# Performance work log

Measured on AMD Instinct MI355X. Metric: run time of the kernel, lower is better.

The kernel has to match this reference:

```python
import jax, jax.numpy as jnp
import numpy as np

B, CAP, H, NH = 128, 65536, 512, 8
HD = H // NH
GH = H // 4  # gate hidden


def setup_inputs() -> dict:
    key = jax.random.key(0)
    ks = jax.random.split(key, 8)
    s = 1.0 / np.sqrt(H)
    sg = 1.0 / np.sqrt(GH)
    return {
        "query": jax.random.normal(ks[0], (B, H), jnp.float32),
        "memory_keys": jax.random.normal(ks[1], (CAP, H), jnp.float32) * s,
        "memory_values": jax.random.normal(ks[2], (CAP, H), jnp.float32) * s,
        "in_proj_w": jax.random.normal(ks[3], (3 * H, H), jnp.float32) * s,
        "in_proj_b": jnp.zeros((3 * H,), jnp.float32),
        "out_proj_w": jax.random.normal(ks[4], (H, H), jnp.float32) * s,
        "out_proj_b": jnp.zeros((H,), jnp.float32),
        "gate_w1": jax.random.normal(ks[5], (GH, H), jnp.float32) * s,
        "gate_b1": jnp.zeros((GH,), jnp.float32),
        "gate_w2": jax.random.normal(ks[6], (1, GH), jnp.float32) * sg,
        "gate_b2": jnp.zeros((1,), jnp.float32),
        "usage_count": jnp.zeros((CAP,), jnp.float32),
        "last_used": jnp.zeros((CAP,), jnp.float32),
        "step_counter": 1,
    }


def reference(query, memory_keys, memory_values, in_proj_w, in_proj_b,
              out_proj_w, out_proj_b, gate_w1, gate_b1, gate_w2, gate_b2,
              usage_count, last_used, step_counter):
    # nn.MultiheadAttention packed projections: rows [0:H]=Wq, [H:2H]=Wk, [2H:3H]=Wv
    wq, wk, wv = in_proj_w[:H], in_proj_w[H:2 * H], in_proj_w[2 * H:]
    bq, bk, bv = in_proj_b[:H], in_proj_b[H:2 * H], in_proj_b[2 * H:]

    q = (query @ wq.T + bq).reshape(B, NH, HD)           # [B, h, d] (q_len = 1)
    k = (memory_keys @ wk.T + bk).reshape(CAP, NH, HD)   # [C, h, d]
    v = (memory_values @ wv.T + bv).reshape(CAP, NH, HD)  # [C, h, d]

    scores = jnp.einsum('bhd,chd->bhc', q, k) / np.sqrt(HD)  # [B, h, C]
    attn = jax.nn.softmax(scores, axis=-1)
    ctx = jnp.einsum('bhc,chd->bhd', attn, v).reshape(B, H)
    attn_out = ctx @ out_proj_w.T + out_proj_b               # [B, H]

    # usage bookkeeping: attn_weights averaged over heads, then over batch
    avg_attn = attn.mean(axis=(0, 1))                        # [C]
    new_usage = usage_count + avg_attn
    new_last = jnp.where(avg_attn > 1e-3,
                         jnp.float32(step_counter), last_used)

    # gating MLP: Linear -> ReLU -> Linear -> Sigmoid
    gate = jax.nn.sigmoid(
        jax.nn.relu(query @ gate_w1.T + gate_b1) @ gate_w2.T + gate_b2)  # [B, 1]
    memory_output = gate * attn_out                          # [B, H]
    return memory_output, new_usage, new_last
```

## Files before the change

### kernel.cpp

```cpp
#include <hip/hip_runtime.h>
#include <stdint.h>


typedef __bf16 b16x8 __attribute__((ext_vector_type(8)));
typedef float f32x4 __attribute__((ext_vector_type(4)));

static __device__ __forceinline__ unsigned short f2bf(float f) {
  unsigned int u = __float_as_uint(f);
  u = (u + 0x7FFFu + ((u >> 16) & 1u)) >> 16;
  return (unsigned short)u;
}

static __device__ __forceinline__ f32x4 MFMA(b16x8 a, b16x8 b, f32x4 c) {
  return __builtin_amdgcn_mfma_f32_16x16x32_bf16(a, b, c, 0, 0, 0);
}

__global__ void k_convert_w(const float* __restrict__ w, unsigned short* __restrict__ dst) {
  int i = blockIdx.x * 256 + threadIdx.x;
  float4 v = reinterpret_cast<const float4*>(w + 512 * 512)[i];
  ushort4 o;
  o.x = f2bf(v.x); o.y = f2bf(v.y); o.z = f2bf(v.z); o.w = f2bf(v.w);
  reinterpret_cast<ushort4*>(dst)[i] = o;
}

__global__ void k_proj_q(const float* __restrict__ query, const float* __restrict__ w,
                         const float* __restrict__ bias, unsigned short* __restrict__ qout) {
  __shared__ float qs[512];
  int b = blockIdx.x, j = threadIdx.x;
  qs[j] = query[b * 512 + j];
  __syncthreads();
  float acc = bias[j];
  const float4* q4 = reinterpret_cast<const float4*>(qs);
  const float4* w4 = reinterpret_cast<const float4*>(w + j * 512);
#pragma unroll 8
  for (int i = 0; i < 128; ++i) {
    float4 a = q4[i], c = w4[i];
    acc += a.x * c.x + a.y * c.y + a.z * c.z + a.w * c.w;
  }
  qout[b * 512 + j] = f2bf(acc);
}

__global__ void k_gate(const float* __restrict__ query, const float* __restrict__ w1,
                       const float* __restrict__ b1, const float* __restrict__ w2,
                       const float* __restrict__ b2, float* __restrict__ gate) {
  __shared__ float qs[512];
  __shared__ float red[2];
  int b = blockIdx.x, j = threadIdx.x;
  qs[j] = query[b * 512 + j];
  qs[j + 128] = query[b * 512 + j + 128];
  qs[j + 256] = query[b * 512 + j + 256];
  qs[j + 384] = query[b * 512 + j + 384];
  __syncthreads();
  float acc = b1[j];
  const float4* q4 = reinterpret_cast<const float4*>(qs);
  const float4* w4 = reinterpret_cast<const float4*>(w1 + j * 512);
#pragma unroll 8
  for (int i = 0; i < 128; ++i) {
    float4 a = q4[i], c = w4[i];
    acc += a.x * c.x + a.y * c.y + a.z * c.z + a.w * c.w;
  }
  float t = fmaxf(acc, 0.f) * w2[j];
#pragma unroll
  for (int off = 1; off < 64; off <<= 1) t += __shfl_xor(t, off, 64);
  if ((j & 63) == 0) red[j >> 6] = t;
  __syncthreads();
  if (j == 0) {
    float z = red[0] + red[1] + b2[0];
    gate[b] = 1.f / (1.f + __builtin_amdgcn_exp2f(-z * 1.44269504088896f));
  }
}

__global__ __launch_bounds__(512) void k_proj_kv(
    const float* __restrict__ mk, const float* __restrict__ mv,
    const unsigned short* __restrict__ wkb, const unsigned short* __restrict__ wvb,
    const float* __restrict__ in_b,
    unsigned short* __restrict__ kout, unsigned short* __restrict__ vtout) {
  const int isV = blockIdx.y;
  const float* A = isV ? mv : mk;
  const unsigned short* W = isV ? wvb : wkb;
  const float* bias = in_b + (isV ? 1024 : 512);
  const int c0 = blockIdx.x * 64;
  const int tid = threadIdx.x;
  const int w = tid >> 6, ln = tid & 15, g = (tid & 63) >> 4;
  __shared__ __align__(16) unsigned short Al[64 * 32];
  __shared__ __align__(16) unsigned short Wl[512 * 32];

  f32x4 acc[4][4];
#pragma unroll
  for (int m = 0; m < 4; ++m)
#pragma unroll
    for (int n = 0; n < 4; ++n) acc[m][n] = {0.f, 0.f, 0.f, 0.f};

  for (int kk = 0; kk < 16; ++kk) {
    {
      int row = tid >> 3, c4 = (tid & 7) << 2;
      float4 v = *reinterpret_cast<const float4*>(&A[(size_t)(c0 + row) * 512 + kk * 32 + c4]);
      ushort4 o;
      o.x = f2bf(v.x); o.y = f2bf(v.y); o.z = f2bf(v.z); o.w = f2bf(v.w);
      *reinterpret_cast<ushort4*>(&Al[row * 32 + c4]) = o;
    }
#pragma unroll
    for (int i = 0; i < 4; ++i) {
      int fc = i * 512 + tid, row = fc >> 2, part = fc & 3;
      *reinterpret_cast<uint4*>(&Wl[row * 32 + part * 8]) =
          *reinterpret_cast<const uint4*>(&W[(size_t)row * 512 + kk * 32 + part * 8]);
    }
    __syncthreads();
    b16x8 a[4], bb[4];
#pragma unroll
    for (int m = 0; m < 4; ++m)
      a[m] = *reinterpret_cast<const b16x8*>(&Al[(16 * m + ln) * 32 + g * 8]);
#pragma unroll
    for (int n = 0; n < 4; ++n)
      bb[n] = *reinterpret_cast<const b16x8*>(&Wl[(64 * w + 16 * n + ln) * 32 + g * 8]);
#pragma unroll
    for (int m = 0; m < 4; ++m)
#pragma unroll
      for (int n = 0; n < 4; ++n) acc[m][n] = MFMA(a[m], bb[n], acc[m][n]);
    __syncthreads();
  }
  float bj[4];
#pragma unroll
  for (int n = 0; n < 4; ++n) bj[n] = bias[64 * w + 16 * n + ln];
#pragma unroll
  for (int m = 0; m < 4; ++m)
#pragma unroll
    for (int n = 0; n < 4; ++n) {
      int j = 64 * w + 16 * n + ln;
#pragma unroll
      for (int r = 0; r < 4; ++r) {
        int c = c0 + 16 * m + 4 * g + r;
        unsigned short val = f2bf(acc[m][n][r] + bj[n]);
        if (!isV) kout[(size_t)c * 512 + j] = val;
        else      vtout[(size_t)j * 65536 + c] = val;
      }
    }
}

__global__ __launch_bounds__(256) void k_attn1(
    const unsigned short* __restrict__ kb, const unsigned short* __restrict__ vt,
    const unsigned short* __restrict__ qb,
    float* __restrict__ l_ws, float* __restrict__ ctxT) {
  const int h = blockIdx.y, cg = blockIdx.x;
  const int tid = threadIdx.x;
  const int wv = tid >> 6, wr = wv >> 1, wc = wv & 1;
  const int ln = tid & 15, g = (tid & 63) >> 4;
  __shared__ __align__(16) unsigned short kS[128 * 64];
  __shared__ __align__(16) unsigned short pS[128 * 128];
  __shared__ __align__(16) unsigned short vS[64 * 128];
  const float SC = 0.125f * 1.44269504088896f;

  b16x8 qf[4][2];
#pragma unroll
  for (int n = 0; n < 4; ++n)
#pragma unroll
    for (int ks = 0; ks < 2; ++ks) {
      int b = 64 * wc + 16 * n + ln;
      qf[n][ks] = *reinterpret_cast<const b16x8*>(&qb[(size_t)b * 512 + h * 64 + ks * 32 + g * 8]);
    }
  f32x4 pacc[2][4];
#pragma unroll
  for (int m = 0; m < 2; ++m)
#pragma unroll
    for (int n = 0; n < 4; ++n) pacc[m][n] = {0.f, 0.f, 0.f, 0.f};
  float lsum[4] = {0.f, 0.f, 0.f, 0.f};

  for (int it = 0; it < 8; ++it) {
    int c0g = cg * 1024 + it * 128;
#pragma unroll
    for (int i = 0; i < 4; ++i) {
      int fl = i * 256 + tid, row = fl >> 3, p8 = fl & 7;
      uint4 d = *reinterpret_cast<const uint4*>(&kb[(size_t)(c0g + row) * 512 + h * 64 + p8 * 8]);
      *reinterpret_cast<uint4*>(&kS[(row * 8 + (p8 ^ (row & 7))) * 8]) = d;
    }
#pragma unroll
    for (int i = 0; i < 4; ++i) {
      int fl = i * 256 + tid, row = fl >> 4, p16 = fl & 15;
      uint4 d = *reinterpret_cast<const uint4*>(&vt[(size_t)(h * 64 + row) * 65536 + c0g + p16 * 8]);
      *reinterpret_cast<uint4*>(&vS[(row * 16 + (p16 ^ (row & 7))) * 8]) = d;
    }
    __syncthreads();

    f32x4 sacc[4][4];
#pragma unroll
    for (int m = 0; m < 4; ++m)
#pragma unroll
      for (int n = 0; n < 4; ++n) sacc[m][n] = {0.f, 0.f, 0.f, 0.f};
#pragma unroll
    for (int ks = 0; ks < 2; ++ks) {
      b16x8 a[4];
#pragma unroll
      for (int m = 0; m < 4; ++m) {
        int row = 64 * wr + 16 * m + ln;
        a[m] = *reinterpret_cast<const b16x8*>(&kS[(row * 8 + ((ks * 4 + g) ^ (row & 7))) * 8]);
      }
#pragma unroll
      for (int m = 0; m < 4; ++m)
#pragma unroll
        for (int n = 0; n < 4; ++n) sacc[m][n] = MFMA(a[m], qf[n][ks], sacc[m][n]);
    }
#pragma unroll
    for (int m = 0; m < 4; ++m)
#pragma unroll
      for (int n = 0; n < 4; ++n) {
        float p0 = __builtin_amdgcn_exp2f(sacc[m][n][0] * SC);
        float p1 = __builtin_amdgcn_exp2f(sacc[m][n][1] * SC);
        float p2 = __builtin_amdgcn_exp2f(sacc[m][n][2] * SC);
        float p3 = __builtin_amdgcn_exp2f(sacc[m][n][3] * SC);
        lsum[n] += (p0 + p1) + (p2 + p3);
        int b = 64 * wc + 16 * n + ln;
        int c = 64 * wr + 16 * m + 4 * g;
        int base = b * 128 + (((c >> 3) ^ (b & 7)) * 8) + (c & 7);
        ushort2 lo, hi;
        lo.x = f2bf(p0); lo.y = f2bf(p1);
        hi.x = f2bf(p2); hi.y = f2bf(p3);
        *reinterpret_cast<ushort2*>(&pS[base]) = lo;
        *reinterpret_cast<ushort2*>(&pS[base + 2]) = hi;
      }
    __syncthreads();
#pragma unroll
    for (int ks = 0; ks < 4; ++ks) {
      b16x8 av[2], bp[4];
#pragma unroll
      for (int m = 0; m < 2; ++m) {
        int row = 32 * wr + 16 * m + ln;
        av[m] = *reinterpret_cast<const b16x8*>(&vS[(row * 16 + ((ks * 4 + g) ^ (row & 7))) * 8]);
      }
#pragma unroll
      for (int n = 0; n < 4; ++n) {
        int row = 64 * wc + 16 * n + ln;
        bp[n] = *reinterpret_cast<const b16x8*>(&pS[(row * 16 + ((ks * 4 + g) ^ (row & 7))) * 8]);
      }
#pragma unroll
      for (int m = 0; m < 2; ++m)
#pragma unroll
        for (int n = 0; n < 4; ++n) pacc[m][n] = MFMA(av[m], bp[n], pacc[m][n]);
    }
    __syncthreads();
  }
#pragma unroll
  for (int n = 0; n < 4; ++n) {
    float v = lsum[n];
    v += __shfl_xor(v, 16, 64);
    v += __shfl_xor(v, 32, 64);
    if ((tid & 63) < 16) atomicAdd(&l_ws[h * 128 + 64 * wc + 16 * n + ln], v);
  }
#pragma unroll
  for (int m = 0; m < 2; ++m)
#pragma unroll
    for (int n = 0; n < 4; ++n)
#pragma unroll
      for (int r = 0; r < 4; ++r) {
        int d = 32 * wr + 16 * m + 4 * g + r;
        int b = 64 * wc + 16 * n + ln;
        atomicAdd(&ctxT[(h * 64 + d) * 128 + b], pacc[m][n][r]);
      }
}

__global__ __launch_bounds__(256) void k_attn2(
    const unsigned short* __restrict__ kb, const unsigned short* __restrict__ qb,
    const float* __restrict__ l_ws, float* __restrict__ avgA) {
  const int h = blockIdx.y, cg = blockIdx.x;
  const int tid = threadIdx.x;
  const int wv = tid >> 6, wr = wv >> 1, wc = wv & 1;
  const int ln = tid & 15, g = (tid & 63) >> 4;
  __shared__ __align__(16) unsigned short kS[128 * 64];
  __shared__ float wS[128];
  const float SC = 0.125f * 1.44269504088896f;
  if (tid < 128) wS[tid] = 1.f / l_ws[h * 128 + tid];
  b16x8 qf[4][2];
#pragma unroll
  for (int n = 0; n < 4; ++n)
#pragma unroll
    for (int ks = 0; ks < 2; ++ks) {
      int b = 64 * wc + 16 * n + ln;
      qf[n][ks] = *reinterpret_cast<const b16x8*>(&qb[(size_t)b * 512 + h * 64 + ks * 32 + g * 8]);
    }
  __syncthreads();
  float wn[4];
#pragma unroll
  for (int n = 0; n < 4; ++n) wn[n] = wS[64 * wc + 16 * n + ln];

  for (int it = 0; it < 8; ++it) {
    int c0g = cg * 1024 + it * 128;
#pragma unroll
    for (int i = 0; i < 4; ++i) {
      int fl = i * 256 + tid, row = fl >> 3, p8 = fl & 7;
      uint4 d = *reinterpret_cast<const uint4*>(&kb[(size_t)(c0g + row) * 512 + h * 64 + p8 * 8]);
      *reinterpret_cast<uint4*>(&kS[(row * 8 + (p8 ^ (row & 7))) * 8]) = d;
    }
    __syncthreads();
    f32x4 sacc[4][4];
#pragma unroll
    for (int m = 0; m < 4; ++m)
#pragma unroll
      for (int n = 0; n < 4; ++n) sacc[m][n] = {0.f, 0.f, 0.f, 0.f};
#pragma unroll
    for (int ks = 0; ks < 2; ++ks) {
      b16x8 a[4];
#pragma unroll
      for (int m = 0; m < 4; ++m) {
        int row = 64 * wr + 16 * m + ln;
        a[m] = *reinterpret_cast<const b16x8*>(&kS[(row * 8 + ((ks * 4 + g) ^ (row & 7))) * 8]);
      }
#pragma unroll
      for (int m = 0; m < 4; ++m)
#pragma unroll
        for (int n = 0; n < 4; ++n) sacc[m][n] = MFMA(a[m], qf[n][ks], sacc[m][n]);
    }
#pragma unroll
    for (int m = 0; m < 4; ++m) {
      float s0 = 0.f, s1 = 0.f, s2 = 0.f, s3 = 0.f;
#pragma unroll
      for (int n = 0; n < 4; ++n) {
        s0 += __builtin_amdgcn_exp2f(sacc[m][n][0] * SC) * wn[n];
        s1 += __builtin_amdgcn_exp2f(sacc[m][n][1] * SC) * wn[n];
        s2 += __builtin_amdgcn_exp2f(sacc[m][n][2] * SC) * wn[n];
        s3 += __builtin_amdgcn_exp2f(sacc[m][n][3] * SC) * wn[n];
      }
#pragma unroll
      for (int off = 1; off < 16; off <<= 1) {
        s0 += __shfl_xor(s0, off, 64);
        s1 += __shfl_xor(s1, off, 64);
        s2 += __shfl_xor(s2, off, 64);
        s3 += __shfl_xor(s3, off, 64);
      }
      if (ln == 0) {
        int c = c0g + 64 * wr + 16 * m + 4 * g;
        atomicAdd(&avgA[c], s0);
        atomicAdd(&avgA[c + 1], s1);
        atomicAdd(&avgA[c + 2], s2);
        atomicAdd(&avgA[c + 3], s3);
      }
    }
    __syncthreads();
  }
}

__global__ void k_finalize(const float* __restrict__ ctxT, const float* __restrict__ l_ws,
                           const float* __restrict__ wout, const float* __restrict__ bout,
                           const float* __restrict__ gate, float* __restrict__ out) {
  __shared__ float cs[512];
  int b = blockIdx.x, j = threadIdx.x;
  cs[j] = ctxT[j * 128 + b] / l_ws[(j >> 6) * 128 + b];
  __syncthreads();
  float acc = bout[j];
  const float4* c4 = reinterpret_cast<const float4*>(cs);
  const float4* w4 = reinterpret_cast<const float4*>(wout + j * 512);
#pragma unroll 8
  for (int i = 0; i < 128; ++i) {
    float4 a = c4[i], c = w4[i];
    acc += a.x * c.x + a.y * c.y + a.z * c.z + a.w * c.w;
  }
  out[b * 512 + j] = gate[b] * acc;
}

__global__ void k_usage(const float* __restrict__ avgA, const float* __restrict__ usage,
                        const float* __restrict__ last, const int* __restrict__ step,
                        float* __restrict__ out_usage, float* __restrict__ out_last) {
  int c = blockIdx.x * 256 + threadIdx.x;
  float avg = avgA[c] * (1.f / 1024.f);
  out_usage[c] = usage[c] + avg;
  out_last[c] = (avg > 0.001f) ? (float)step[0] : last[c];
}

extern "C" void kernel_launch(void* const* d_in, const int* in_sizes, int n_in,
                              void* d_out, int out_size, void* d_ws, size_t ws_size,
                              hipStream_t stream) {
  const float* query = (const float*)d_in[0];
  const float* mk    = (const float*)d_in[1];
  const float* mv    = (const float*)d_in[2];
  const float* in_w  = (const float*)d_in[3];
  const float* in_b  = (const float*)d_in[4];
  const float* out_w = (const float*)d_in[5];
  const float* out_b = (const float*)d_in[6];
  const float* gw1   = (const float*)d_in[7];
  const float* gb1   = (const float*)d_in[8];
  const float* gw2   = (const float*)d_in[9];
  const float* gb2   = (const float*)d_in[10];
  const float* usage = (const float*)d_in[11];
  const float* last  = (const float*)d_in[12];
  const int*   step  = (const int*)d_in[13];

  char* ws = (char*)d_ws;
  unsigned short* qb  = (unsigned short*)(ws);
  unsigned short* wkb = (unsigned short*)(ws + 131072);
  unsigned short* wvb = (unsigned short*)(ws + 655360);
  unsigned short* kb  = (unsigned short*)(ws + 1179648);
  unsigned short* vt  = (unsigned short*)(ws + 68288512);
  float* l_ws = (float*)(ws + 135397376);
  float* ctxT = (float*)(ws + 135401472);
  float* avgA = (float*)(ws + 135663616);
  float* gate = (float*)(ws + 135925760);
  float* out = (float*)d_out;

  hipMemsetAsync(ws + 135397376, 0, 4096 + 262144 + 262144, stream);

  k_convert_w<<<512, 256, 0, stream>>>(in_w, wkb);
  k_proj_q<<<128, 512, 0, stream>>>(query, in_w, in_b, qb);
  k_gate<<<128, 128, 0, stream>>>(query, gw1, gb1, gw2, gb2, gate);
  k_proj_kv<<<dim3(1024, 2), 512, 0, stream>>>(mk, mv, wkb, wvb, in_b, kb, vt);
  k_attn1<<<dim3(64, 8), 256, 0, stream>>>(kb, vt, qb, l_ws, ctxT);
  k_attn2<<<dim3(64, 8), 256, 0, stream>>>(kb, qb, l_ws, avgA);
  k_finalize<<<128, 512, 0, stream>>>(ctxT, l_ws, out_w, out_b, gate, out);
  k_usage<<<256, 256, 0, stream>>>(avgA, usage, last, step, out + 65536, out + 131072);
}
```

Baseline: 413.3 us.

## Retile K/V projection into 128x128 tiles with direct-to-LDS weight loads and swizzle

The K/V projection GEMM now uses 128x128 output tiles with 256 threads instead of 64 rows by the full 512 columns with 512 threads. Weight tiles are loaded straight into LDS with global_load_lds, and both LDS tiles use an XOR swizzle to avoid bank conflicts. The transposed V output is written as 4-element vector stores. The memory rows are now re-read and re-converted once per column tile (4x), trading extra fp32 input traffic for smaller LDS use and higher occupancy.

```diff
diff --git a/kernel.cpp b/kernel.cpp
--- a/kernel.cpp
+++ b/kernel.cpp
@@ -4,6 +4,7 @@
 
 typedef __bf16 b16x8 __attribute__((ext_vector_type(8)));
 typedef float f32x4 __attribute__((ext_vector_type(4)));
+typedef unsigned short u16x8 __attribute__((ext_vector_type(8)));
 
 static __device__ __forceinline__ unsigned short f2bf(float f) {
   unsigned int u = __float_as_uint(f);
@@ -14,6 +15,11 @@
 static __device__ __forceinline__ f32x4 MFMA(b16x8 a, b16x8 b, f32x4 c) {
   return __builtin_amdgcn_mfma_f32_16x16x32_bf16(a, b, c, 0, 0, 0);
 }
+
+#define GLL16(g, l)                                                          \
+  __builtin_amdgcn_global_load_lds(                                          \
+      (const __attribute__((address_space(1))) void*)(g),                    \
+      (__attribute__((address_space(3))) void*)(l), 16, 0, 0)
 
 __global__ void k_convert_w(const float* __restrict__ w, unsigned short* __restrict__ dst) {
   int i = blockIdx.x * 256 + threadIdx.x;
@@ -70,20 +76,24 @@
   }
 }
 
-__global__ __launch_bounds__(512) void k_proj_kv(
+__global__ __launch_bounds__(256) void k_proj_kv(
     const float* __restrict__ mk, const float* __restrict__ mv,
     const unsigned short* __restrict__ wkb, const unsigned short* __restrict__ wvb,
     const float* __restrict__ in_b,
     unsigned short* __restrict__ kout, unsigned short* __restrict__ vtout) {
-  const int isV = blockIdx.y;
-  const float* A = isV ? mv : mk;
+  const int isV = blockIdx.z;
+  const float* Ag = isV ? mv : mk;
   const unsigned short* W = isV ? wvb : wkb;
   const float* bias = in_b + (isV ? 1024 : 512);
-  const int c0 = blockIdx.x * 64;
+  const int j0 = blockIdx.x * 128;
+  const int c0 = blockIdx.y * 128;
   const int tid = threadIdx.x;
-  const int w = tid >> 6, ln = tid & 15, g = (tid & 63) >> 4;
-  __shared__ __align__(16) unsigned short Al[64 * 32];
-  __shared__ __align__(16) unsigned short Wl[512 * 32];
+  const int wv = tid >> 6, wr = wv >> 1, wc = wv & 1;
+  const int ln = tid & 15, g = (tid & 63) >> 4;
+  const int sw = (ln >> 1) & 3;
+
+  __shared__ __align__(16) unsigned short Al[128 * 32];
+  __shared__ __align__(16) unsigned short Wl[128 * 32];
 
   f32x4 acc[4][4];
 #pragma unroll
@@ -91,48 +101,73 @@
 #pragma unroll
     for (int n = 0; n < 4; ++n) acc[m][n] = {0.f, 0.f, 0.f, 0.f};
 
+  const int arow = tid >> 1, ah = tid & 1;
+  const float* aptr = Ag + (size_t)(c0 + arow) * 512 + ah * 16;
+  const int s_a = (arow >> 1) & 3;
+  unsigned short* awr0 = &Al[arow * 32 + (((2 * ah) ^ s_a) << 3)];
+  unsigned short* awr1 = &Al[arow * 32 + (((2 * ah + 1) ^ s_a) << 3)];
+
+  const int r0 = tid >> 2, p0 = (tid & 3) ^ ((r0 >> 1) & 3);
+  const int r1 = 64 + (tid >> 2), p1 = (tid & 3) ^ ((r1 >> 1) & 3);
+  const unsigned short* wsrc0 = W + (size_t)(j0 + r0) * 512 + p0 * 8;
+  const unsigned short* wsrc1 = W + (size_t)(j0 + r1) * 512 + p1 * 8;
+  unsigned short* wdst0 = &Wl[(wv << 6) * 8];
+  unsigned short* wdst1 = &Wl[(256 + (wv << 6)) * 8];
+
   for (int kk = 0; kk < 16; ++kk) {
-    {
-      int row = tid >> 3, c4 = (tid & 7) << 2;
-      float4 v = *reinterpret_cast<const float4*>(&A[(size_t)(c0 + row) * 512 + kk * 32 + c4]);
-      ushort4 o;
-      o.x = f2bf(v.x); o.y = f2bf(v.y); o.z = f2bf(v.z); o.w = f2bf(v.w);
-      *reinterpret_cast<ushort4*>(&Al[row * 32 + c4]) = o;
-    }
-#pragma unroll
-    for (int i = 0; i < 4; ++i) {
-      int fc = i * 512 + tid, row = fc >> 2, part = fc & 3;
-      *reinterpret_cast<uint4*>(&Wl[row * 32 + part * 8]) =
-          *reinterpret_cast<const uint4*>(&W[(size_t)row * 512 + kk * 32 + part * 8]);
-    }
-    __syncthreads();
-    b16x8 a[4], bb[4];
+    GLL16(wsrc0 + kk * 32, wdst0);
+    GLL16(wsrc1 + kk * 32, wdst1);
+    const float4* ap = reinterpret_cast<const float4*>(aptr + kk * 32);
+    float4 f0 = ap[0], f1 = ap[1], f2 = ap[2], f3 = ap[3];
+    u16x8 lo, hi;
+    lo[0] = f2bf(f0.x); lo[1] = f2bf(f0.y); lo[2] = f2bf(f0.z); lo[3] = f2bf(f0.w);
+    lo[4] = f2bf(f1.x); lo[5] = f2bf(f1.y); lo[6] = f2bf(f1.z); lo[7] = f2bf(f1.w);
+    hi[0] = f2bf(f2.x); hi[1] = f2bf(f2.y); hi[2] = f2bf(f2.z); hi[3] = f2bf(f2.w);
+    hi[4] = f2bf(f3.x); hi[5] = f2bf(f3.y); hi[6] = f2bf(f3.z); hi[7] = f2bf(f3.w);
+    *reinterpret_cast<u16x8*>(awr0) = lo;
+    *reinterpret_cast<u16x8*>(awr1) = hi;
+    __syncthreads();
+
+    b16x8 af[4], wf[4];
+#pragma unroll
+    for (int m = 0; m < 4; ++m) {
+      int row = 64 * wr + 16 * m + ln;
+      af[m] = *reinterpret_cast<const b16x8*>(&Al[row * 32 + ((g ^ sw) << 3)]);
+    }
+#pragma unroll
+    for (int n = 0; n < 4; ++n) {
+      int row = 64 * wc + 16 * n + ln;
+      wf[n] = *reinterpret_cast<const b16x8*>(&Wl[row * 32 + ((g ^ sw) << 3)]);
+    }
 #pragma unroll
     for (int m = 0; m < 4; ++m)
-      a[m] = *reinterpret_cast<const b16x8*>(&Al[(16 * m + ln) * 32 + g * 8]);
-#pragma unroll
-    for (int n = 0; n < 4; ++n)
-      bb[n] = *reinterpret_cast<const b16x8*>(&Wl[(64 * w + 16 * n + ln) * 32 + g * 8]);
-#pragma unroll
-    for (int m = 0; m < 4; ++m)
-#pragma unroll
-      for (int n = 0; n < 4; ++n) acc[m][n] = MFMA(a[m], bb[n], acc[m][n]);
-    __syncthreads();
-  }
+#pragma unroll
+      for (int n = 0; n < 4; ++n) acc[m][n] = MFMA(af[m], wf[n], acc[m][n]);
+    __syncthreads();
+  }
+
   float bj[4];
 #pragma unroll
-  for (int n = 0; n < 4; ++n) bj[n] = bias[64 * w + 16 * n + ln];
+  for (int n = 0; n < 4; ++n) bj[n] = bias[j0 + 64 * wc + 16 * n + ln];
 #pragma unroll
   for (int m = 0; m < 4; ++m)
 #pragma unroll
     for (int n = 0; n < 4; ++n) {
-      int j = 64 * w + 16 * n + ln;
-#pragma unroll
-      for (int r = 0; r < 4; ++r) {
-        int c = c0 + 16 * m + 4 * g + r;
-        unsigned short val = f2bf(acc[m][n][r] + bj[n]);
-        if (!isV) kout[(size_t)c * 512 + j] = val;
-        else      vtout[(size_t)j * 65536 + c] = val;
+      int j = j0 + 64 * wc + 16 * n + ln;
+      if (!isV) {
+#pragma unroll
+        for (int r = 0; r < 4; ++r) {
+          int c = c0 + 64 * wr + 16 * m + 4 * g + r;
+          kout[(size_t)c * 512 + j] = f2bf(acc[m][n][r] + bj[n]);
+        }
+      } else {
+        ushort4 o;
+        o.x = f2bf(acc[m][n][0] + bj[n]);
+        o.y = f2bf(acc[m][n][1] + bj[n]);
+        o.z = f2bf(acc[m][n][2] + bj[n]);
+        o.w = f2bf(acc[m][n][3] + bj[n]);
+        int c = c0 + 64 * wr + 16 * m + 4 * g;
+        *reinterpret_cast<ushort4*>(&vtout[(size_t)j * 65536 + c]) = o;
       }
     }
 }
@@ -399,7 +434,7 @@
   k_convert_w<<<512, 256, 0, stream>>>(in_w, wkb);
   k_proj_q<<<128, 512, 0, stream>>>(query, in_w, in_b, qb);
   k_gate<<<128, 128, 0, stream>>>(query, gw1, gb1, gw2, gb2, gate);
-  k_proj_kv<<<dim3(1024, 2), 512, 0, stream>>>(mk, mv, wkb, wvb, in_b, kb, vt);
+  k_proj_kv<<<dim3(4, 512, 2), 256, 0, stream>>>(mk, mv, wkb, wvb, in_b, kb, vt);
   k_attn1<<<dim3(64, 8), 256, 0, stream>>>(kb, vt, qb, l_ws, ctxT);
   k_attn2<<<dim3(64, 8), 256, 0, stream>>>(kb, qb, l_ws, avgA);
   k_finalize<<<128, 512, 0, stream>>>(ctxT, l_ws, out_w, out_b, gate, out);
```

New measurement: 414.1 us. Within noise of the previous version (+0.2%).
